# Kernel optimization log

Hardware: AMD Instinct MI355X
Metric: run time of the kernel (lower is better)

The kernel has to match this reference:

```python
import jax, jax.numpy as jnp
import numpy as np

N_NODES = 40000
N_EDGES = 640000
IN_FEATS = 128
HID = 64
# layer widths per GCN.__init__: in->h->2h->2h->h->h->h->1
DIMS = [IN_FEATS, HID, 2 * HID, 2 * HID, HID, HID, HID, 1]


def setup_inputs() -> dict:
    key = jax.random.key(0)
    ks = jax.random.split(key, 3 + 2 * 7)
    inp = {
        "in_feat": jax.random.normal(ks[0], (N_NODES, IN_FEATS), dtype=jnp.float32),
        "src": jax.random.randint(ks[1], (N_EDGES,), 0, N_NODES, dtype=jnp.int32),
        "dst": jax.random.randint(ks[2], (N_EDGES,), 0, N_NODES, dtype=jnp.int32),
    }
    # DGL GraphConv params: weight [in, out] (glorot), bias [out] (zeros; use small randn for a nontrivial baseline)
    for i in range(7):
        din, dout = DIMS[i], DIMS[i + 1]
        scale = jnp.sqrt(6.0 / (din + dout)).astype(jnp.float32)
        inp[f"W{i+1}"] = jax.random.uniform(ks[3 + 2 * i], (din, dout), jnp.float32, -scale, scale)
        inp[f"b{i+1}"] = 0.01 * jax.random.normal(ks[4 + 2 * i], (dout,), dtype=jnp.float32)
    return inp


def _graph_conv(x, W, b, src, dst, out_norm, in_norm, n_nodes):
    # DGL GraphConv, norm='both', allow_zero_in_degree=True:
    #   h = D_in^{-1/2} * A^T * (D_out^{-1/2} * x) @ W + b
    x = x * out_norm[:, None]
    if x.shape[1] > W.shape[1]:
        # mult W first to shrink message dim (mirrors DGL's heuristic; math-equivalent)
        x = x @ W
        h = jax.ops.segment_sum(x[src], dst, num_segments=n_nodes)
    else:
        h = jax.ops.segment_sum(x[src], dst, num_segments=n_nodes)
        h = h @ W
    return h * in_norm[:, None] + b


def reference(in_feat, src, dst, W1, b1, W2, b2, W3, b3, W4, b4, W5, b5, W6, b6, W7, b7):
    n = in_feat.shape[0]
    ones = jnp.ones((src.shape[0],), dtype=jnp.float32)
    out_deg = jax.ops.segment_sum(ones, src, num_segments=n)
    in_deg = jax.ops.segment_sum(ones, dst, num_segments=n)
    out_norm = jnp.where(out_deg > 0, jax.lax.rsqrt(jnp.maximum(out_deg, 1.0)), 0.0)
    in_norm = jnp.where(in_deg > 0, jax.lax.rsqrt(jnp.maximum(in_deg, 1.0)), 0.0)

    params = [(W1, b1), (W2, b2), (W3, b3), (W4, b4), (W5, b5), (W6, b6), (W7, b7)]
    h = in_feat
    for i, (W, b) in enumerate(params):
        h = _graph_conv(h, W, b, src, dst, out_norm, in_norm, n)
        if i < 6:
            h = jax.nn.relu(h)
    return h  # [N, 1]
```

## Files before the change

kernel.cpp:

```cpp
#include <hip/hip_runtime.h>
#include <hip/hip_bf16.h>


#define IN_F 128
#define NSLICE 60
#define SHB 13
#define NSHARD 5

typedef __attribute__((ext_vector_type(8))) short short8v;
typedef __attribute__((ext_vector_type(4))) float f32x4;
typedef __attribute__((ext_vector_type(8))) _Float16 half8v;

static __device__ __forceinline__ unsigned short f2bf(float x) {
    unsigned u = __builtin_bit_cast(unsigned, x);
    unsigned r = (u + 0x7FFFu + ((u >> 16) & 1u)) >> 16;
    return (unsigned short)r;
}
static __device__ __forceinline__ float bf2f(unsigned short h) {
    unsigned u = ((unsigned)h) << 16;
    return __builtin_bit_cast(float, u);
}


__global__ __launch_bounds__(256) void hist2_kernel(const int* __restrict__ src,
                                                    const int* __restrict__ dst,
                                                    int* __restrict__ scratch, int E) {
    constexpr int SH = 1 << SHB;
    __shared__ int h[SH];
    const int t = threadIdx.x;
    const int b = blockIdx.x;
    const int s = blockIdx.y;
    const int z = blockIdx.z;
    const int* idx = z ? dst : src;
    for (int i = t; i < SH; i += 256) h[i] = 0;
    __syncthreads();
    const int per = (E + NSLICE - 1) / NSLICE;
    const int lo = b * per;
    const int hiE = min(lo + per, E);
    const int base = s << SHB;
    for (int e = lo + t; e < hiE; e += 256) {
        unsigned a = (unsigned)(idx[e] - base);
        if (a < (unsigned)SH) atomicAdd(&h[a], 1);
    }
    __syncthreads();
    int* so = scratch + ((size_t)((z * NSHARD + s) * NSLICE + b) << SHB);
    for (int i = t; i < SH; i += 256) so[i] = h[i];
}

__global__ void hist_reduce_kernel(const int* __restrict__ scratch,
                                   int* __restrict__ in_deg,
                                   float* __restrict__ out_nrm,
                                   float* __restrict__ in_nrm, int N) {
    constexpr int SH = 1 << SHB;
    int n = blockIdx.x * blockDim.x + threadIdx.x;
    if (n >= N) return;
    int s = n >> SHB;
    int i = n & (SH - 1);
    int od = 0, idg = 0;
    for (int b = 0; b < NSLICE; ++b) {
        od  += scratch[((size_t)((0 * NSHARD + s) * NSLICE + b) << SHB) + i];
        idg += scratch[((size_t)((1 * NSHARD + s) * NSLICE + b) << SHB) + i];
    }
    in_deg[n] = idg;
    out_nrm[n] = od  > 0 ? rsqrtf((float)od)  : 0.f;
    in_nrm[n]  = idg > 0 ? rsqrtf((float)idg) : 0.f;
}


__global__ __launch_bounds__(256) void scan_blk_kernel(const int* __restrict__ deg,
                                                       int* __restrict__ blockSums, int N) {
    __shared__ int ws[4];
    const int t = threadIdx.x;
    const int base = blockIdx.x * 1024 + t * 4;
    int4 v = make_int4(0, 0, 0, 0);
    if (base + 3 < N) v = *reinterpret_cast<const int4*>(&deg[base]);
    else if (base < N) {
        v.x = deg[base];
        if (base + 1 < N) v.y = deg[base + 1];
        if (base + 2 < N) v.z = deg[base + 2];
    }
    int s = v.x + v.y + v.z + v.w;
#pragma unroll
    for (int off = 32; off > 0; off >>= 1) s += __shfl_down(s, off);
    if ((t & 63) == 0) ws[t >> 6] = s;
    __syncthreads();
    if (t == 0) blockSums[blockIdx.x] = ws[0] + ws[1] + ws[2] + ws[3];
}

__global__ __launch_bounds__(64) void scan_top_kernel(const int* __restrict__ blockSums,
                                                      int* __restrict__ blockOffs,
                                                      int* __restrict__ row_off, int NB, int N) {
    const int t = threadIdx.x;
    int orig = (t < NB) ? blockSums[t] : 0;
    int v = orig;
#pragma unroll
    for (int off = 1; off < 64; off <<= 1) {
        int u = __shfl_up(v, off);
        if (t >= off) v += u;
    }
    if (t < NB) blockOffs[t] = v - orig;
    if (t == 63) row_off[N] = v;
}

__global__ __launch_bounds__(256) void scan_fill_kernel(const int* __restrict__ deg,
                                                        const int* __restrict__ blockOffs,
                                                        int* __restrict__ row_off, int N) {
    __shared__ int wtot[4];
    const int t = threadIdx.x;
    const int lane = t & 63;
    const int wid = t >> 6;
    const int base = blockIdx.x * 1024 + t * 4;
    int4 v = make_int4(0, 0, 0, 0);
    if (base + 3 < N) v = *reinterpret_cast<const int4*>(&deg[base]);
    else if (base < N) {
        v.x = deg[base];
        if (base + 1 < N) v.y = deg[base + 1];
        if (base + 2 < N) v.z = deg[base + 2];
    }
    const int s = v.x + v.y + v.z + v.w;
    int incl = s;
#pragma unroll
    for (int off = 1; off < 64; off <<= 1) {
        int u = __shfl_up(incl, off);
        if (lane >= off) incl += u;
    }
    if (lane == 63) wtot[wid] = incl;
    __syncthreads();
    int pre = blockOffs[blockIdx.x] + incl - s;
    for (int i = 0; i < wid; ++i) pre += wtot[i];
    if (base < N) {
        int run = pre;
        row_off[base] = run; run += v.x;
        if (base + 1 < N) { row_off[base + 1] = run; run += v.y; }
        if (base + 2 < N) { row_off[base + 2] = run; run += v.z; }
        if (base + 3 < N) { row_off[base + 3] = run; }
    }
}

__global__ void slice_base_kernel(int* __restrict__ scratch,
                                  const int* __restrict__ row_off, int N) {
    constexpr int SH = 1 << SHB;
    int n = blockIdx.x * blockDim.x + threadIdx.x;
    if (n >= N) return;
    int s = n >> SHB;
    int i = n & (SH - 1);
    int run = row_off[n];
    for (int b = 0; b < NSLICE; ++b) {
        size_t off = ((size_t)((NSHARD + s) * NSLICE + b) << SHB) + i;
        int c = scratch[off];
        scratch[off] = run;
        run += c;
    }
}

__global__ __launch_bounds__(256) void fill2_kernel(const int* __restrict__ src,
                                                    const int* __restrict__ dst,
                                                    const int* __restrict__ scratch,
                                                    int* __restrict__ csr, int E) {
    constexpr int SH = 1 << SHB;
    __shared__ int cur[SH];
    const int t = threadIdx.x;
    const int b = blockIdx.x;
    const int s = blockIdx.y;
    const int* base = scratch + ((size_t)((NSHARD + s) * NSLICE + b) << SHB);
    for (int i = t; i < SH; i += 256) cur[i] = base[i];
    __syncthreads();
    const int per = (E + NSLICE - 1) / NSLICE;
    const int lo = b * per;
    const int hiE = min(lo + per, E);
    const int nb = s << SHB;
    for (int e = lo + t; e < hiE; e += 256) {
        unsigned a = (unsigned)(dst[e] - nb);
        if (a < (unsigned)SH) {
            int pos = atomicAdd(&cur[a], 1);
            csr[pos] = src[e];
        }
    }
}


__global__ void split_feat_kernel(const float* __restrict__ x, const float* __restrict__ snrm,
                                  unsigned short* __restrict__ th, unsigned short* __restrict__ tl,
                                  int total4) {
    int i = blockIdx.x * blockDim.x + threadIdx.x;
    if (i >= total4) return;
    float4 v = reinterpret_cast<const float4*>(x)[i];
    float sc = snrm[i >> 5];
    ushort4 h, l;
    float a;
    a = v.x * sc; h.x = f2bf(a); l.x = f2bf(a - bf2f(h.x));
    a = v.y * sc; h.y = f2bf(a); l.y = f2bf(a - bf2f(h.y));
    a = v.z * sc; h.z = f2bf(a); l.z = f2bf(a - bf2f(h.z));
    a = v.w * sc; h.w = f2bf(a); l.w = f2bf(a - bf2f(h.w));
    reinterpret_cast<ushort4*>(th)[i] = h;
    reinterpret_cast<ushort4*>(tl)[i] = l;
}

struct WDesc { const float* w; unsigned short* th; unsigned short* tl; int K; int N; };
struct WPack { WDesc d[6]; };

__global__ __launch_bounds__(256) void split_w_kernel(WPack p) {
    WDesc d = p.d[blockIdx.x];
    int i = blockIdx.y * 256 + threadIdx.x;
    if (i >= d.K * d.N) return;
    int k = i / d.N, n = i - k * d.N;
    float v = d.w[i];
    unsigned short h = f2bf(v);
    d.th[(size_t)n * d.K + k] = h;
    d.tl[(size_t)n * d.K + k] = f2bf(v - bf2f(h));
}


template<int K, int NOUT, bool POST, bool RELU, bool POST2, int OUTM>
__global__ __launch_bounds__(256) void gemm_mfma(
    const unsigned short* __restrict__ Ah, const unsigned short* __restrict__ Al,
    const unsigned short* __restrict__ Bh, const unsigned short* __restrict__ Bl,
    const float* __restrict__ r_nrm, const float* __restrict__ s_nrm,
    const float* __restrict__ bias,
    _Float16* __restrict__ Y16, unsigned short* __restrict__ Yh,
    unsigned short* __restrict__ Yl, int M) {
    constexpr int NT = NOUT / 16;
    const int lane = threadIdx.x & 63;
    const int wv = threadIdx.x >> 6;
    const int r0 = blockIdx.x * 64 + wv * 16;
    const int arow = r0 + (lane & 15);
    const int kg = (lane >> 4) * 8;

    f32x4 acc[NT];
#pragma unroll
    for (int n = 0; n < NT; ++n) acc[n] = (f32x4){0.f, 0.f, 0.f, 0.f};

    for (int kk = 0; kk < K; kk += 32) {
        short8v a_h = *reinterpret_cast<const short8v*>(Ah + (size_t)arow * K + kk + kg);
        short8v a_l = *reinterpret_cast<const short8v*>(Al + (size_t)arow * K + kk + kg);
#pragma unroll
        for (int n = 0; n < NT; ++n) {
            int col = n * 16 + (lane & 15);
            short8v b_h = *reinterpret_cast<const short8v*>(Bh + (size_t)col * K + kk + kg);
            short8v b_l = *reinterpret_cast<const short8v*>(Bl + (size_t)col * K + kk + kg);
            acc[n] = __builtin_amdgcn_mfma_f32_16x16x32_bf16(a_h, b_h, acc[n], 0, 0, 0);
            acc[n] = __builtin_amdgcn_mfma_f32_16x16x32_bf16(a_h, b_l, acc[n], 0, 0, 0);
            acc[n] = __builtin_amdgcn_mfma_f32_16x16x32_bf16(a_l, b_h, acc[n], 0, 0, 0);
        }
    }

    const int c0 = lane & 15;
    const int rr = r0 + (lane >> 4) * 4;
#pragma unroll
    for (int n = 0; n < NT; ++n) {
        const int col = n * 16 + c0;
        const float bcol = POST ? bias[col] : 0.f;
#pragma unroll
        for (int j = 0; j < 4; ++j) {
            const int row = rr + j;
            float y = acc[n][j];
            if (POST) y = fmaf(y, r_nrm[row], bcol);
            if (RELU) y = fmaxf(y, 0.f);
            if (POST2) y *= s_nrm[row];
            if (OUTM == 0) {
                Y16[(size_t)row * NOUT + col] = (_Float16)y;
            } else {
                unsigned short h = f2bf(y);
                Yh[(size_t)row * NOUT + col] = h;
                Yl[(size_t)row * NOUT + col] = f2bf(y - bf2f(h));
            }
        }
    }
}


template<int F, bool POST, bool RELU, bool POST2, int OUTM>
__global__ __launch_bounds__(256) void agg_h16(
    const _Float16* __restrict__ X, const int* __restrict__ csr,
    const int* __restrict__ row_off, const float* __restrict__ r_nrm,
    const float* __restrict__ s_nrm, const float* __restrict__ bias,
    _Float16* __restrict__ Y16, unsigned short* __restrict__ Yh,
    unsigned short* __restrict__ Yl, int N) {
    constexpr int LPE = F / 8;
    constexpr int EPW = 64 / LPE;
    const int lane = threadIdx.x & 63;
    const int node = blockIdx.x * (blockDim.x >> 6) + (threadIdx.x >> 6);
    if (node >= N) return;
    const int g = lane / LPE;
    const int c = lane % LPE;
    const int lo = row_off[node];
    const int hi = row_off[node + 1];
    float acc[8], acc2[8];
#pragma unroll
    for (int j = 0; j < 8; ++j) { acc[j] = 0.f; acc2[j] = 0.f; }
    int e = lo + g;
    for (; e + EPW < hi; e += 2 * EPW) {
        int s0 = csr[e];
        int s1 = csr[e + EPW];
        half8v x0 = *reinterpret_cast<const half8v*>(&X[(size_t)s0 * F + c * 8]);
        half8v x1 = *reinterpret_cast<const half8v*>(&X[(size_t)s1 * F + c * 8]);
#pragma unroll
        for (int j = 0; j < 8; ++j) { acc[j] += (float)x0[j]; acc2[j] += (float)x1[j]; }
    }
    if (e < hi) {
        int s0 = csr[e];
        half8v x0 = *reinterpret_cast<const half8v*>(&X[(size_t)s0 * F + c * 8]);
#pragma unroll
        for (int j = 0; j < 8; ++j) acc[j] += (float)x0[j];
    }
#pragma unroll
    for (int j = 0; j < 8; ++j) acc[j] += acc2[j];
#pragma unroll
    for (int m = LPE; m < 64; m <<= 1) {
#pragma unroll
        for (int j = 0; j < 8; ++j) acc[j] += __shfl_xor(acc[j], m);
    }
    if (lane < LPE) {
        if (POST) {
            float rn = r_nrm[node];
#pragma unroll
            for (int j = 0; j < 8; ++j) acc[j] = fmaf(acc[j], rn, bias[lane * 8 + j]);
        }
        if (RELU) {
#pragma unroll
            for (int j = 0; j < 8; ++j) acc[j] = fmaxf(acc[j], 0.f);
        }
        if (POST2) {
            float sn = s_nrm[node];
#pragma unroll
            for (int j = 0; j < 8; ++j) acc[j] *= sn;
        }
        if (OUTM == 0) {
            half8v o;
#pragma unroll
            for (int j = 0; j < 8; ++j) o[j] = (_Float16)acc[j];
            *reinterpret_cast<half8v*>(&Y16[(size_t)node * F + lane * 8]) = o;
        } else {
            short8v h, l;
#pragma unroll
            for (int j = 0; j < 8; ++j) {
                unsigned short hh = f2bf(acc[j]);
                h[j] = (short)hh;
                l[j] = (short)f2bf(acc[j] - bf2f(hh));
            }
            *reinterpret_cast<short8v*>(&Yh[(size_t)node * F + lane * 8]) = h;
            *reinterpret_cast<short8v*>(&Yl[(size_t)node * F + lane * 8]) = l;
        }
    }
}


__global__ __launch_bounds__(256) void gemv64_kernel(const _Float16* __restrict__ X,
                                                     const float* __restrict__ W,
                                                     float* __restrict__ Y, int M) {
    const int lane = threadIdx.x & 63;
    const int m = blockIdx.x * (blockDim.x >> 6) + (threadIdx.x >> 6);
    if (m >= M) return;
    float v = (float)X[(size_t)m * 64 + lane] * W[lane];
#pragma unroll
    for (int off = 32; off > 0; off >>= 1) v += __shfl_down(v, off);
    if (lane == 0) Y[m] = v;
}

__global__ __launch_bounds__(256) void agg1_kernel(const float* __restrict__ T,
                                                   const int* __restrict__ csr,
                                                   const int* __restrict__ row_off,
                                                   const float* __restrict__ r_nrm,
                                                   const float* __restrict__ bias,
                                                   float* __restrict__ Y, int N) {
    const int node = blockIdx.x * 16 + (threadIdx.x >> 4);
    const int l = threadIdx.x & 15;
    if (node >= N) return;
    const int lo = row_off[node];
    const int hi = row_off[node + 1];
    float acc = 0.f;
    for (int e = lo + l; e < hi; e += 16) acc += T[csr[e]];
#pragma unroll
    for (int m = 8; m >= 1; m >>= 1) acc += __shfl_xor(acc, m);
    if (l == 0) Y[node] = fmaf(acc, r_nrm[node], bias[0]);
}


extern "C" void kernel_launch(void* const* d_in, const int* in_sizes, int n_in,
                              void* d_out, int out_size, void* d_ws, size_t ws_size,
                              hipStream_t stream) {
    const float* in_feat = (const float*)d_in[0];
    const int* src = (const int*)d_in[1];
    const int* dst = (const int*)d_in[2];
    const float* W1 = (const float*)d_in[3];  const float* B1 = (const float*)d_in[4];
    const float* W2 = (const float*)d_in[5];  const float* B2 = (const float*)d_in[6];
    const float* W3 = (const float*)d_in[7];  const float* B3 = (const float*)d_in[8];
    const float* W4 = (const float*)d_in[9];  const float* B4 = (const float*)d_in[10];
    const float* W5 = (const float*)d_in[11]; const float* B5 = (const float*)d_in[12];
    const float* W6 = (const float*)d_in[13]; const float* B6 = (const float*)d_in[14];
    const float* W7 = (const float*)d_in[15]; const float* B7 = (const float*)d_in[16];

    const int N = in_sizes[0] / IN_F;
    const int E = in_sizes[1];
    float* out = (float*)d_out;

    char* w = (char*)d_ws;
    auto alloc = [&](size_t bytes) { char* p = w; w += (bytes + 255) & ~(size_t)255; return p; };
    int* csr      = (int*)alloc((size_t)E * 4);
    int* row_off  = (int*)alloc((size_t)(N + 1) * 4);
    int* in_deg   = (int*)alloc((size_t)N * 4);
    int* blockSums= (int*)alloc(64 * 4);
    int* blockOffs= (int*)alloc(64 * 4);
    float* out_nrm= (float*)alloc((size_t)N * 4);
    float* in_nrm = (float*)alloc((size_t)N * 4);
    float* t7     = (float*)alloc((size_t)N * 4);
    const int dims[8] = {128, 64, 128, 128, 64, 64, 64, 1};
    unsigned short* wth[6]; unsigned short* wtl[6];
    for (int i = 0; i < 6; ++i) {
        size_t kn = (size_t)dims[i] * dims[i + 1];
        wth[i] = (unsigned short*)alloc(kn * 2);
        wtl[i] = (unsigned short*)alloc(kn * 2);
    }
    unsigned short* fh = (unsigned short*)alloc((size_t)N * 128 * 2);
    unsigned short* fl = (unsigned short*)alloc((size_t)N * 128 * 2);
    unsigned short* th = (unsigned short*)alloc((size_t)N * 128 * 2);
    unsigned short* tl = (unsigned short*)alloc((size_t)N * 128 * 2);
    _Float16* h0 = (_Float16*)alloc((size_t)N * 128 * 2);
    _Float16* h1 = (_Float16*)alloc((size_t)N * 128 * 2);
    int* scratch = (int*)fh;
    (void)ws_size; (void)n_in; (void)out_size;

    const int TB = 256;
    const int NB = (N + 1023) / 1024;

    WPack wp;
    const float* Ws[6] = {W1, W2, W3, W4, W5, W6};
    for (int i = 0; i < 6; ++i) wp.d[i] = {Ws[i], wth[i], wtl[i], dims[i], dims[i + 1]};
    split_w_kernel<<<dim3(6, 64), TB, 0, stream>>>(wp);

    hist2_kernel<<<dim3(NSLICE, NSHARD, 2), TB, 0, stream>>>(src, dst, scratch, E);
    hist_reduce_kernel<<<(N + TB - 1) / TB, TB, 0, stream>>>(
        scratch, in_deg, out_nrm, in_nrm, N);
    scan_blk_kernel<<<NB, TB, 0, stream>>>(in_deg, blockSums, N);
    scan_top_kernel<<<1, 64, 0, stream>>>(blockSums, blockOffs, row_off, NB, N);
    scan_fill_kernel<<<NB, TB, 0, stream>>>(in_deg, blockOffs, row_off, N);
    slice_base_kernel<<<(N + TB - 1) / TB, TB, 0, stream>>>(scratch, row_off, N);
    fill2_kernel<<<dim3(NSLICE, NSHARD), TB, 0, stream>>>(src, dst, scratch, csr, E);

    split_feat_kernel<<<(N * 32 + TB - 1) / TB, TB, 0, stream>>>(
        in_feat, out_nrm, fh, fl, N * 32);

    const int gridN4 = (N + 3) / 4;
    const int MB = N / 64;

    gemm_mfma<128, 64, false, false, false, 0><<<MB, TB, 0, stream>>>(
        fh, fl, wth[0], wtl[0], nullptr, nullptr, nullptr, h0, nullptr, nullptr, N);
    agg_h16<64, true, true, true, 0><<<gridN4, TB, 0, stream>>>(
        h0, csr, row_off, in_nrm, out_nrm, B1, h1, nullptr, nullptr, N);

    agg_h16<64, false, false, false, 1><<<gridN4, TB, 0, stream>>>(
        h1, csr, row_off, nullptr, nullptr, nullptr, nullptr, th, tl, N);
    gemm_mfma<64, 128, true, true, true, 0><<<MB, TB, 0, stream>>>(
        th, tl, wth[1], wtl[1], in_nrm, out_nrm, B2, h0, nullptr, nullptr, N);

    agg_h16<128, false, false, false, 1><<<gridN4, TB, 0, stream>>>(
        h0, csr, row_off, nullptr, nullptr, nullptr, nullptr, th, tl, N);
    gemm_mfma<128, 128, true, true, true, 1><<<MB, TB, 0, stream>>>(
        th, tl, wth[2], wtl[2], in_nrm, out_nrm, B3, nullptr, fh, fl, N);

    gemm_mfma<128, 64, false, false, false, 0><<<MB, TB, 0, stream>>>(
        fh, fl, wth[3], wtl[3], nullptr, nullptr, nullptr, h0, nullptr, nullptr, N);
    agg_h16<64, true, true, true, 0><<<gridN4, TB, 0, stream>>>(
        h0, csr, row_off, in_nrm, out_nrm, B4, h1, nullptr, nullptr, N);

    agg_h16<64, false, false, false, 1><<<gridN4, TB, 0, stream>>>(
        h1, csr, row_off, nullptr, nullptr, nullptr, nullptr, th, tl, N);
    gemm_mfma<64, 64, true, true, true, 0><<<MB, TB, 0, stream>>>(
        th, tl, wth[4], wtl[4], in_nrm, out_nrm, B5, h0, nullptr, nullptr, N);

    agg_h16<64, false, false, false, 1><<<gridN4, TB, 0, stream>>>(
        h0, csr, row_off, nullptr, nullptr, nullptr, nullptr, th, tl, N);
    gemm_mfma<64, 64, true, true, true, 0><<<MB, TB, 0, stream>>>(
        th, tl, wth[5], wtl[5], in_nrm, out_nrm, B6, h1, nullptr, nullptr, N);

    gemv64_kernel<<<gridN4, TB, 0, stream>>>(h1, W7, t7, N);
    agg1_kernel<<<(N + 15) / 16, TB, 0, stream>>>(t7, csr, row_off, in_nrm, B7, out, N);
}
```

Baseline: 310.2 us.

## Fuse neighbor aggregation with MFMA GEMM and fold input split into GEMM

Adds a fused kernel that aggregates neighbor features for 64 nodes into LDS as bf16 hi/lo pairs, using an XOR swizzle to avoid bank conflicts, then runs the split-bf16 MFMA GEMM with bias, ReLU and norm epilogue directly. This removes the intermediate th/tl round trip through global memory and one launch per layer for layers 2, 3, 5 and 6. The first layer's GEMM now reads the fp32 input and does the norm scaling and hi/lo split in registers, which drops the separate split_feat pass. The cost is lower parallelism in the gather: one wave now serially processes 16 nodes instead of one node per wave, and the LDS use limits occupancy.

```diff
diff --git a/kernel.cpp b/kernel.cpp
--- a/kernel.cpp
+++ b/kernel.cpp
@@ -179,23 +179,6 @@
 }
 
 
-__global__ void split_feat_kernel(const float* __restrict__ x, const float* __restrict__ snrm,
-                                  unsigned short* __restrict__ th, unsigned short* __restrict__ tl,
-                                  int total4) {
-    int i = blockIdx.x * blockDim.x + threadIdx.x;
-    if (i >= total4) return;
-    float4 v = reinterpret_cast<const float4*>(x)[i];
-    float sc = snrm[i >> 5];
-    ushort4 h, l;
-    float a;
-    a = v.x * sc; h.x = f2bf(a); l.x = f2bf(a - bf2f(h.x));
-    a = v.y * sc; h.y = f2bf(a); l.y = f2bf(a - bf2f(h.y));
-    a = v.z * sc; h.z = f2bf(a); l.z = f2bf(a - bf2f(h.z));
-    a = v.w * sc; h.w = f2bf(a); l.w = f2bf(a - bf2f(h.w));
-    reinterpret_cast<ushort4*>(th)[i] = h;
-    reinterpret_cast<ushort4*>(tl)[i] = l;
-}
-
 struct WDesc { const float* w; unsigned short* th; unsigned short* tl; int K; int N; };
 struct WPack { WDesc d[6]; };
 
@@ -211,28 +194,36 @@
 }
 
 
-template<int K, int NOUT, bool POST, bool RELU, bool POST2, int OUTM>
-__global__ __launch_bounds__(256) void gemm_mfma(
-    const unsigned short* __restrict__ Ah, const unsigned short* __restrict__ Al,
+template<int K, int NOUT>
+__global__ __launch_bounds__(256) void gemm_mfma_f32(
+    const float* __restrict__ X,
     const unsigned short* __restrict__ Bh, const unsigned short* __restrict__ Bl,
-    const float* __restrict__ r_nrm, const float* __restrict__ s_nrm,
-    const float* __restrict__ bias,
-    _Float16* __restrict__ Y16, unsigned short* __restrict__ Yh,
-    unsigned short* __restrict__ Yl, int M) {
+    const float* __restrict__ pre, _Float16* __restrict__ Y16, int M) {
     constexpr int NT = NOUT / 16;
     const int lane = threadIdx.x & 63;
     const int wv = threadIdx.x >> 6;
     const int r0 = blockIdx.x * 64 + wv * 16;
     const int arow = r0 + (lane & 15);
     const int kg = (lane >> 4) * 8;
+    const float sc = pre[arow];
 
     f32x4 acc[NT];
 #pragma unroll
     for (int n = 0; n < NT; ++n) acc[n] = (f32x4){0.f, 0.f, 0.f, 0.f};
 
     for (int kk = 0; kk < K; kk += 32) {
-        short8v a_h = *reinterpret_cast<const short8v*>(Ah + (size_t)arow * K + kk + kg);
-        short8v a_l = *reinterpret_cast<const short8v*>(Al + (size_t)arow * K + kk + kg);
+        const float* ap = &X[(size_t)arow * K + kk + kg];
+        float4 v0 = *reinterpret_cast<const float4*>(ap);
+        float4 v1 = *reinterpret_cast<const float4*>(ap + 4);
+        float a[8] = {v0.x, v0.y, v0.z, v0.w, v1.x, v1.y, v1.z, v1.w};
+        short8v a_h, a_l;
+#pragma unroll
+        for (int j = 0; j < 8; ++j) {
+            float f = a[j] * sc;
+            unsigned short hh = f2bf(f);
+            a_h[j] = (short)hh;
+            a_l[j] = (short)f2bf(f - bf2f(hh));
+        }
 #pragma unroll
         for (int n = 0; n < NT; ++n) {
             int col = n * 16 + (lane & 15);
@@ -243,20 +234,160 @@
             acc[n] = __builtin_amdgcn_mfma_f32_16x16x32_bf16(a_l, b_h, acc[n], 0, 0, 0);
         }
     }
-
     const int c0 = lane & 15;
     const int rr = r0 + (lane >> 4) * 4;
 #pragma unroll
     for (int n = 0; n < NT; ++n) {
         const int col = n * 16 + c0;
-        const float bcol = POST ? bias[col] : 0.f;
+#pragma unroll
+        for (int j = 0; j < 4; ++j)
+            Y16[(size_t)(rr + j) * NOUT + col] = (_Float16)acc[n][j];
+    }
+}
+
+
+template<int K, int NOUT>
+__global__ __launch_bounds__(256) void gemm_mfma(
+    const unsigned short* __restrict__ Ah, const unsigned short* __restrict__ Al,
+    const unsigned short* __restrict__ Bh, const unsigned short* __restrict__ Bl,
+    _Float16* __restrict__ Y16, int M) {
+    constexpr int NT = NOUT / 16;
+    const int lane = threadIdx.x & 63;
+    const int wv = threadIdx.x >> 6;
+    const int r0 = blockIdx.x * 64 + wv * 16;
+    const int arow = r0 + (lane & 15);
+    const int kg = (lane >> 4) * 8;
+
+    f32x4 acc[NT];
+#pragma unroll
+    for (int n = 0; n < NT; ++n) acc[n] = (f32x4){0.f, 0.f, 0.f, 0.f};
+
+    for (int kk = 0; kk < K; kk += 32) {
+        short8v a_h = *reinterpret_cast<const short8v*>(Ah + (size_t)arow * K + kk + kg);
+        short8v a_l = *reinterpret_cast<const short8v*>(Al + (size_t)arow * K + kk + kg);
+#pragma unroll
+        for (int n = 0; n < NT; ++n) {
+            int col = n * 16 + (lane & 15);
+            short8v b_h = *reinterpret_cast<const short8v*>(Bh + (size_t)col * K + kk + kg);
+            short8v b_l = *reinterpret_cast<const short8v*>(Bl + (size_t)col * K + kk + kg);
+            acc[n] = __builtin_amdgcn_mfma_f32_16x16x32_bf16(a_h, b_h, acc[n], 0, 0, 0);
+            acc[n] = __builtin_amdgcn_mfma_f32_16x16x32_bf16(a_h, b_l, acc[n], 0, 0, 0);
+            acc[n] = __builtin_amdgcn_mfma_f32_16x16x32_bf16(a_l, b_h, acc[n], 0, 0, 0);
+        }
+    }
+    const int c0 = lane & 15;
+    const int rr = r0 + (lane >> 4) * 4;
+#pragma unroll
+    for (int n = 0; n < NT; ++n) {
+        const int col = n * 16 + c0;
+#pragma unroll
+        for (int j = 0; j < 4; ++j)
+            Y16[(size_t)(rr + j) * NOUT + col] = (_Float16)acc[n][j];
+    }
+}
+
+
+template<int K, int NOUT, int OUTM>
+__global__ __launch_bounds__(256) void fused_ag(
+    const _Float16* __restrict__ X, const int* __restrict__ csr,
+    const int* __restrict__ row_off,
+    const unsigned short* __restrict__ Bh, const unsigned short* __restrict__ Bl,
+    const float* __restrict__ r_nrm, const float* __restrict__ s_nrm,
+    const float* __restrict__ bias,
+    _Float16* __restrict__ Y16, unsigned short* __restrict__ Yh,
+    unsigned short* __restrict__ Yl, int N) {
+    constexpr int G = K / 8;
+    constexpr int LPE = G;
+    constexpr int EPW = 64 / LPE;
+    constexpr int NT = NOUT / 16;
+    __shared__ unsigned short sAh[64 * K];
+    __shared__ unsigned short sAl[64 * K];
+    const int lane = threadIdx.x & 63;
+    const int wv = threadIdx.x >> 6;
+    const int g = lane / LPE;
+    const int c = lane % LPE;
+    const int nodeBase = blockIdx.x * 64 + wv * 16;
+
+    for (int i = 0; i < 16; ++i) {
+        const int node = nodeBase + i;
+        if (node >= N) break;
+        const int lo = row_off[node];
+        const int hi = row_off[node + 1];
+        float acc[8], acc2[8];
+#pragma unroll
+        for (int j = 0; j < 8; ++j) { acc[j] = 0.f; acc2[j] = 0.f; }
+        int e = lo + g;
+        for (; e + EPW < hi; e += 2 * EPW) {
+            int s0 = csr[e];
+            int s1 = csr[e + EPW];
+            half8v x0 = *reinterpret_cast<const half8v*>(&X[(size_t)s0 * K + c * 8]);
+            half8v x1 = *reinterpret_cast<const half8v*>(&X[(size_t)s1 * K + c * 8]);
+#pragma unroll
+            for (int j = 0; j < 8; ++j) { acc[j] += (float)x0[j]; acc2[j] += (float)x1[j]; }
+        }
+        if (e < hi) {
+            int s0 = csr[e];
+            half8v x0 = *reinterpret_cast<const half8v*>(&X[(size_t)s0 * K + c * 8]);
+#pragma unroll
+            for (int j = 0; j < 8; ++j) acc[j] += (float)x0[j];
+        }
+#pragma unroll
+        for (int j = 0; j < 8; ++j) acc[j] += acc2[j];
+#pragma unroll
+        for (int m = LPE; m < 64; m <<= 1) {
+#pragma unroll
+            for (int j = 0; j < 8; ++j) acc[j] += __shfl_xor(acc[j], m);
+        }
+        if (lane < LPE) {
+            const int row = wv * 16 + i;
+            short8v hv, lv;
+#pragma unroll
+            for (int j = 0; j < 8; ++j) {
+                unsigned short hh = f2bf(acc[j]);
+                hv[j] = (short)hh;
+                lv[j] = (short)f2bf(acc[j] - bf2f(hh));
+            }
+            const int grp = c ^ (row & (G - 1));
+            *reinterpret_cast<short8v*>(&sAh[row * K + grp * 8]) = hv;
+            *reinterpret_cast<short8v*>(&sAl[row * K + grp * 8]) = lv;
+        }
+    }
+    __syncthreads();
+
+    const int arow = wv * 16 + (lane & 15);
+    f32x4 oacc[NT];
+#pragma unroll
+    for (int n = 0; n < NT; ++n) oacc[n] = (f32x4){0.f, 0.f, 0.f, 0.f};
+
+    for (int kk = 0; kk < K; kk += 32) {
+        const int gidx = (kk >> 3) + (lane >> 4);
+        const int grp = gidx ^ (arow & (G - 1));
+        short8v a_h = *reinterpret_cast<const short8v*>(&sAh[arow * K + grp * 8]);
+        short8v a_l = *reinterpret_cast<const short8v*>(&sAl[arow * K + grp * 8]);
+        const int kg = (lane >> 4) * 8;
+#pragma unroll
+        for (int n = 0; n < NT; ++n) {
+            int col = n * 16 + (lane & 15);
+            short8v b_h = *reinterpret_cast<const short8v*>(Bh + (size_t)col * K + kk + kg);
+            short8v b_l = *reinterpret_cast<const short8v*>(Bl + (size_t)col * K + kk + kg);
+            oacc[n] = __builtin_amdgcn_mfma_f32_16x16x32_bf16(a_h, b_h, oacc[n], 0, 0, 0);
+            oacc[n] = __builtin_amdgcn_mfma_f32_16x16x32_bf16(a_h, b_l, oacc[n], 0, 0, 0);
+            oacc[n] = __builtin_amdgcn_mfma_f32_16x16x32_bf16(a_l, b_h, oacc[n], 0, 0, 0);
+        }
+    }
+
+    const int c0 = lane & 15;
+    const int rr = blockIdx.x * 64 + wv * 16 + (lane >> 4) * 4;
+#pragma unroll
+    for (int n = 0; n < NT; ++n) {
+        const int col = n * 16 + c0;
+        const float bcol = bias[col];
 #pragma unroll
         for (int j = 0; j < 4; ++j) {
             const int row = rr + j;
-            float y = acc[n][j];
-            if (POST) y = fmaf(y, r_nrm[row], bcol);
-            if (RELU) y = fmaxf(y, 0.f);
-            if (POST2) y *= s_nrm[row];
+            float y = fmaf(oacc[n][j], r_nrm[row], bcol);
+            y = fmaxf(y, 0.f);
+            y *= s_nrm[row];
             if (OUTM == 0) {
                 Y16[(size_t)row * NOUT + col] = (_Float16)y;
             } else {
@@ -269,13 +400,12 @@
 }
 
 
-template<int F, bool POST, bool RELU, bool POST2, int OUTM>
+template<int F>
 __global__ __launch_bounds__(256) void agg_h16(
     const _Float16* __restrict__ X, const int* __restrict__ csr,
     const int* __restrict__ row_off, const float* __restrict__ r_nrm,
     const float* __restrict__ s_nrm, const float* __restrict__ bias,
-    _Float16* __restrict__ Y16, unsigned short* __restrict__ Yh,
-    unsigned short* __restrict__ Yl, int N) {
+    _Float16* __restrict__ Y16, int N) {
     constexpr int LPE = F / 8;
     constexpr int EPW = 64 / LPE;
     const int lane = threadIdx.x & 63;
@@ -311,36 +441,16 @@
         for (int j = 0; j < 8; ++j) acc[j] += __shfl_xor(acc[j], m);
     }
     if (lane < LPE) {
-        if (POST) {
-            float rn = r_nrm[node];
-#pragma unroll
-            for (int j = 0; j < 8; ++j) acc[j] = fmaf(acc[j], rn, bias[lane * 8 + j]);
-        }
-        if (RELU) {
-#pragma unroll
-            for (int j = 0; j < 8; ++j) acc[j] = fmaxf(acc[j], 0.f);
-        }
-        if (POST2) {
-            float sn = s_nrm[node];
-#pragma unroll
-            for (int j = 0; j < 8; ++j) acc[j] *= sn;
-        }
-        if (OUTM == 0) {
-            half8v o;
-#pragma unroll
-            for (int j = 0; j < 8; ++j) o[j] = (_Float16)acc[j];
-            *reinterpret_cast<half8v*>(&Y16[(size_t)node * F + lane * 8]) = o;
-        } else {
-            short8v h, l;
-#pragma unroll
-            for (int j = 0; j < 8; ++j) {
-                unsigned short hh = f2bf(acc[j]);
-                h[j] = (short)hh;
-                l[j] = (short)f2bf(acc[j] - bf2f(hh));
-            }
-            *reinterpret_cast<short8v*>(&Yh[(size_t)node * F + lane * 8]) = h;
-            *reinterpret_cast<short8v*>(&Yl[(size_t)node * F + lane * 8]) = l;
-        }
+        float rn = r_nrm[node];
+        float sn = s_nrm[node];
+        half8v o;
+#pragma unroll
+        for (int j = 0; j < 8; ++j) {
+            float y = fmaf(acc[j], rn, bias[lane * 8 + j]);
+            y = fmaxf(y, 0.f) * sn;
+            o[j] = (_Float16)y;
+        }
+        *reinterpret_cast<half8v*>(&Y16[(size_t)node * F + lane * 8]) = o;
     }
 }
 
@@ -411,13 +521,11 @@
         wth[i] = (unsigned short*)alloc(kn * 2);
         wtl[i] = (unsigned short*)alloc(kn * 2);
     }
-    unsigned short* fh = (unsigned short*)alloc((size_t)N * 128 * 2);
-    unsigned short* fl = (unsigned short*)alloc((size_t)N * 128 * 2);
     unsigned short* th = (unsigned short*)alloc((size_t)N * 128 * 2);
     unsigned short* tl = (unsigned short*)alloc((size_t)N * 128 * 2);
     _Float16* h0 = (_Float16*)alloc((size_t)N * 128 * 2);
     _Float16* h1 = (_Float16*)alloc((size_t)N * 128 * 2);
-    int* scratch = (int*)fh;
+    int* scratch = (int*)th;
     (void)ws_size; (void)n_in; (void)out_size;
 
     const int TB = 256;
@@ -437,42 +545,27 @@
     slice_base_kernel<<<(N + TB - 1) / TB, TB, 0, stream>>>(scratch, row_off, N);
     fill2_kernel<<<dim3(NSLICE, NSHARD), TB, 0, stream>>>(src, dst, scratch, csr, E);
 
-    split_feat_kernel<<<(N * 32 + TB - 1) / TB, TB, 0, stream>>>(
-        in_feat, out_nrm, fh, fl, N * 32);
-
     const int gridN4 = (N + 3) / 4;
-    const int MB = N / 64;
-
-    gemm_mfma<128, 64, false, false, false, 0><<<MB, TB, 0, stream>>>(
-        fh, fl, wth[0], wtl[0], nullptr, nullptr, nullptr, h0, nullptr, nullptr, N);
-    agg_h16<64, true, true, true, 0><<<gridN4, TB, 0, stream>>>(
-        h0, csr, row_off, in_nrm, out_nrm, B1, h1, nullptr, nullptr, N);
-
-    agg_h16<64, false, false, false, 1><<<gridN4, TB, 0, stream>>>(
-        h1, csr, row_off, nullptr, nullptr, nullptr, nullptr, th, tl, N);
-    gemm_mfma<64, 128, true, true, true, 0><<<MB, TB, 0, stream>>>(
-        th, tl, wth[1], wtl[1], in_nrm, out_nrm, B2, h0, nullptr, nullptr, N);
-
-    agg_h16<128, false, false, false, 1><<<gridN4, TB, 0, stream>>>(
-        h0, csr, row_off, nullptr, nullptr, nullptr, nullptr, th, tl, N);
-    gemm_mfma<128, 128, true, true, true, 1><<<MB, TB, 0, stream>>>(
-        th, tl, wth[2], wtl[2], in_nrm, out_nrm, B3, nullptr, fh, fl, N);
-
-    gemm_mfma<128, 64, false, false, false, 0><<<MB, TB, 0, stream>>>(
-        fh, fl, wth[3], wtl[3], nullptr, nullptr, nullptr, h0, nullptr, nullptr, N);
-    agg_h16<64, true, true, true, 0><<<gridN4, TB, 0, stream>>>(
-        h0, csr, row_off, in_nrm, out_nrm, B4, h1, nullptr, nullptr, N);
-
-    agg_h16<64, false, false, false, 1><<<gridN4, TB, 0, stream>>>(
-        h1, csr, row_off, nullptr, nullptr, nullptr, nullptr, th, tl, N);
-    gemm_mfma<64, 64, true, true, true, 0><<<MB, TB, 0, stream>>>(
-        th, tl, wth[4], wtl[4], in_nrm, out_nrm, B5, h0, nullptr, nullptr, N);
-
-    agg_h16<64, false, false, false, 1><<<gridN4, TB, 0, stream>>>(
-        h0, csr, row_off, nullptr, nullptr, nullptr, nullptr, th, tl, N);
-    gemm_mfma<64, 64, true, true, true, 0><<<MB, TB, 0, stream>>>(
-        th, tl, wth[5], wtl[5], in_nrm, out_nrm, B6, h1, nullptr, nullptr, N);
-
-    gemv64_kernel<<<gridN4, TB, 0, stream>>>(h1, W7, t7, N);
+    const int MB = (N + 63) / 64;
+
+    gemm_mfma_f32<128, 64><<<MB, TB, 0, stream>>>(in_feat, wth[0], wtl[0], out_nrm, h0, N);
+    agg_h16<64><<<gridN4, TB, 0, stream>>>(h0, csr, row_off, in_nrm, out_nrm, B1, h1, N);
+
+    fused_ag<64, 128, 0><<<MB, TB, 0, stream>>>(
+        h1, csr, row_off, wth[1], wtl[1], in_nrm, out_nrm, B2, h0, nullptr, nullptr, N);
+
+    fused_ag<128, 128, 1><<<MB, TB, 0, stream>>>(
+        h0, csr, row_off, wth[2], wtl[2], in_nrm, out_nrm, B3, nullptr, th, tl, N);
+
+    gemm_mfma<128, 64><<<MB, TB, 0, stream>>>(th, tl, wth[3], wtl[3], h1, N);
+    agg_h16<64><<<gridN4, TB, 0, stream>>>(h1, csr, row_off, in_nrm, out_nrm, B4, h0, N);
+
+    fused_ag<64, 64, 0><<<MB, TB, 0, stream>>>(
+        h0, csr, row_off, wth[4], wtl[4], in_nrm, out_nrm, B5, h1, nullptr, nullptr, N);
+
+    fused_ag<64, 64, 0><<<MB, TB, 0, stream>>>(
+        h1, csr, row_off, wth[5], wtl[5], in_nrm, out_nrm, B6, h0, nullptr, nullptr, N);
+
+    gemv64_kernel<<<gridN4, TB, 0, stream>>>(h0, W7, t7, N);
     agg1_kernel<<<(N + 15) / 16, TB, 0, stream>>>(t7, csr, row_off, in_nrm, B7, out, N);
 }
```

Result: slower. 347.9 us (+12.2%).
